# Kernel tuning notes

Hardware: AMD Instinct MI355X
Metric: run time of the kernel (lower is better)

## Reference

```python
import jax, jax.numpy as jnp
import numpy as np

B, S, D, H, BLK = 2, 4096, 1024, 16, 64

def setup_inputs() -> dict:
    key = jax.random.key(0)
    ks = jax.random.split(key, 6)
    sc = 0.02
    nb = S // BLK
    g_tok = 128
    ng = g_tok // BLK
    n_mid = nb - ng - 2
    return {
        "tokens": jax.random.normal(ks[0], (B, S, D), dtype=jnp.float32),
        "band_mask": jnp.ones((B, 1, n_mid, BLK, 3 * BLK), dtype=jnp.float32),
        "from_mask": jnp.ones((B, 1, S, 1), dtype=jnp.float32),
        "to_mask": jnp.ones((B, 1, 1, S), dtype=jnp.float32),
        "Wq": jax.random.normal(ks[1], (D, D), dtype=jnp.float32) * sc,
        "Wk": jax.random.normal(ks[2], (D, D), dtype=jnp.float32) * sc,
        "Wv": jax.random.normal(ks[3], (D, D), dtype=jnp.float32) * sc,
        "Wu": jax.random.normal(ks[4], (D, D), dtype=jnp.float32) * sc,
        "bu": jnp.zeros((D,), dtype=jnp.float32),
        "num_global_tokens": 128,
    }

def _forward(tokens, band_mask, from_mask, to_mask, Wq, Wk, Wv, Wu, bu, g):
    b, s, dm = tokens.shape
    h, blk = H, BLK
    d = dm // h
    nb = s // blk
    ng = g // blk
    rs = 1.0 / (d ** 0.5)
    pen = -10000.0

    def heads(x):
        return x.reshape(b, s, h, d).transpose(0, 2, 1, 3)  # (b,h,s,d)

    q = heads(tokens @ Wq)
    k = heads(tokens @ Wk)
    v = heads(tokens @ Wv)
    bq = q.reshape(b, h, nb, blk, d)
    bk = k.reshape(b, h, nb, blk, d)
    bv = v.reshape(b, h, nb, blk, d)

    # --- global (first) block rows: attend to everything ---
    fp = jnp.einsum('bhqd,bhkd->bhqk', q[:, :, :g], k) * rs + (1.0 - to_mask) * pen
    fw = jax.nn.softmax(fp, axis=-1)
    first = jnp.einsum('bhqk,bhkd->bhqd', fw, v).reshape(b, h, ng, blk, d)

    # --- second block: global keys + first 3 non-global blocks ---
    q1 = min(3, nb - ng)
    st = ng * blk
    k2 = jnp.concatenate([k[:, :, :g], k[:, :, st:st + q1 * blk]], axis=2)
    v2 = jnp.concatenate([v[:, :, :g], v[:, :, st:st + q1 * blk]], axis=2)
    p2 = jnp.einsum('bhqd,bhkd->bhqk', bq[:, :, ng], k2) * rs
    p2 = p2 + (1.0 - to_mask[:, :, :, :blk * (ng + q1)]) * pen
    c2 = jnp.einsum('bhqk,bhkd->bhqd', jax.nn.softmax(p2, axis=-1), v2)[:, :, None]

    # --- middle blocks: sliding window (prev, self, next) + global keys ---
    m = nb - ng - 2
    ek = jnp.concatenate([bk[:, :, ng:ng + m], bk[:, :, ng + 1:ng + 1 + m],
                          bk[:, :, ng + 2:ng + 2 + m]], axis=3)  # (b,h,m,3*blk,d)
    ev = jnp.concatenate([bv[:, :, ng:ng + m], bv[:, :, ng + 1:ng + 1 + m],
                          bv[:, :, ng + 2:ng + 2 + m]], axis=3)
    mq = bq[:, :, ng + 1:ng + 1 + m]  # (b,h,m,blk,d)
    inner = jnp.einsum('bhmqd,bhmkd->bhmqk', mq, ek) * rs + (1.0 - band_mask) * pen
    fb = jnp.einsum('bhmqd,bhkd->bhmqk', mq, k[:, :, :g]) * rs
    fb = fb + (1.0 - to_mask[:, :, :, :g][:, :, :, None, :]) * pen
    aw = jax.nn.softmax(jnp.concatenate([fb, inner], axis=-1), axis=-1)
    cm = (jnp.einsum('bhmqk,bhmkd->bhmqd', aw[..., g:], ev)
          + jnp.einsum('bhmqk,bhkd->bhmqd', aw[..., :g], v[:, :, :g]))

    # --- last block: global keys + last 3 blocks ---
    ql = min(3, nb - ng)
    kl = jnp.concatenate([k[:, :, :g], k[:, :, -(ql * blk):]], axis=2)
    vl = jnp.concatenate([v[:, :, :g], v[:, :, -(ql * blk):]], axis=2)
    lm = jnp.concatenate([to_mask[:, :, :, :g], to_mask[:, :, :, -(ql * blk):]], axis=3)
    pl = jnp.einsum('bhqd,bhkd->bhqk', bq[:, :, -1], kl) * rs + (1.0 - lm) * pen
    cl = jnp.einsum('bhqk,bhkd->bhqd', jax.nn.softmax(pl, axis=-1), vl)[:, :, None]

    ctx = jnp.concatenate([first, c2, cm, cl], axis=2).reshape(b, h, s, d) * from_mask
    ctx = ctx.transpose(0, 2, 1, 3).reshape(b, s, dm)
    return ctx @ Wu + bu

def reference(tokens, band_mask, from_mask, to_mask, Wq, Wk, Wv, Wu, bu, num_global_tokens):
    return _forward(tokens, band_mask, from_mask, to_mask, Wq, Wk, Wv, Wu, bu, num_global_tokens)
```

## Files before the change

### kernel.cpp

```cpp
#include <hip/hip_runtime.h>

typedef unsigned short u16;
using bfrag = __attribute__((ext_vector_type(8))) short;
using f32x4 = __attribute__((ext_vector_type(4))) float;

#define PEN  (-10000.0f)
#define RSC  (0.125f)

__device__ __forceinline__ u16 f2bf(float f) {
  union { float f; unsigned u; } v; v.f = f;
  unsigned r = v.u + 0x7fffu + ((v.u >> 16) & 1u);
  return (u16)(r >> 16);
}

__device__ __forceinline__ void gload16(const u16* g, u16* l) {
  __builtin_amdgcn_global_load_lds(
      (const __attribute__((address_space(1))) unsigned int*)g,
      (__attribute__((address_space(3))) unsigned int*)l, 16, 0, 0);
}

__global__ __launch_bounds__(256) void prep_k(
    const float* __restrict__ tokens, u16* __restrict__ tok_bf,
    const float* __restrict__ w0, const float* __restrict__ w1,
    const float* __restrict__ w2, const float* __restrict__ w3,
    u16* __restrict__ wt) {
  __shared__ float tile[64][65];
  int id = blockIdx.x, t = threadIdx.x;
  if (id < 8192) {
    int i = id * 256 + t;
    float4 v = ((const float4*)tokens)[i];
    u16 o[4] = { f2bf(v.x), f2bf(v.y), f2bf(v.z), f2bf(v.w) };
    *(uint2*)(tok_bf + (size_t)i * 4) = *(uint2*)o;
    return;
  }
  int wid = id - 8192;
  int z = wid >> 8, rem = wid & 255;
  const float* W = (z == 0) ? w0 : (z == 1) ? w1 : (z == 2) ? w2 : w3;
  u16* out = wt + (size_t)z * 1024 * 1024;
  int k0 = (rem & 15) * 64, n0 = (rem >> 4) * 64;
#pragma unroll
  for (int i = 0; i < 16; ++i) {
    int idx = i * 256 + t, kk = idx >> 6, nn = idx & 63;
    tile[nn][kk] = W[(size_t)(k0 + kk) * 1024 + n0 + nn];
  }
  __syncthreads();
#pragma unroll
  for (int i = 0; i < 16; ++i) {
    int idx = i * 256 + t, nn = idx >> 6, kk = idx & 63;
    out[(size_t)(n0 + nn) * 1024 + k0 + kk] = f2bf(tile[nn][kk]);
  }
}

__global__ __launch_bounds__(256) void gemm_qkv_k(
    const u16* __restrict__ A, const u16* __restrict__ WT,
    u16* __restrict__ Q, u16* __restrict__ K, u16* __restrict__ VT) {
  __shared__ alignas(16) u16 smem[17408];
  u16* As = smem;
  u16* Bs = smem + 8192;
  int t = threadIdx.x;
  int n0 = blockIdx.x * 128, r0 = blockIdx.y * 128;
  int wave = t >> 6, lane = t & 63, quad = lane >> 4, lcol = lane & 15;
  int wr = wave & 1, wc = wave >> 1;
  int rsel = lane >> 3;
  int sseg = (lane & 7) ^ rsel;
  f32x4 acc[4][4];
#pragma unroll
  for (int mt = 0; mt < 4; ++mt)
#pragma unroll
    for (int nt = 0; nt < 4; ++nt) acc[mt][nt] = (f32x4){0.f, 0.f, 0.f, 0.f};

  const u16* a0 = A + (size_t)r0 * 1024 + sseg * 8;
  const u16* b0 = WT + (size_t)n0 * 1024 + sseg * 8;
  int sw = lcol & 7;

  for (int kt = 0; kt < 16; ++kt) {
#pragma unroll
    for (int i = 0; i < 4; ++i) {
      int ii = wave * 4 + i;
      int row = ii * 8 + rsel;
      gload16(a0 + (size_t)row * 1024 + kt * 64, As + ii * 512);
      gload16(b0 + (size_t)row * 1024 + kt * 64, Bs + ii * 512);
    }
    __syncthreads();
#pragma unroll
    for (int kh = 0; kh < 2; ++kh) {
      int seg = ((kh * 4 + quad) ^ sw) * 8;
      bfrag af[4], bf[4];
#pragma unroll
      for (int x = 0; x < 4; ++x) {
        af[x] = *(const bfrag*)(As + (wr * 64 + x * 16 + lcol) * 64 + seg);
        bf[x] = *(const bfrag*)(Bs + (wc * 64 + x * 16 + lcol) * 64 + seg);
      }
#pragma unroll
      for (int mt = 0; mt < 4; ++mt)
#pragma unroll
        for (int nt = 0; nt < 4; ++nt)
          acc[mt][nt] = __builtin_amdgcn_mfma_f32_16x16x32_bf16(af[mt], bf[nt], acc[mt][nt], 0, 0, 0);
    }
    __syncthreads();
  }
  u16 (*Cs)[136] = (u16(*)[136])smem;
#pragma unroll
  for (int mt = 0; mt < 4; ++mt)
#pragma unroll
    for (int nt = 0; nt < 4; ++nt)
#pragma unroll
      for (int r = 0; r < 4; ++r)
        Cs[wr * 64 + mt * 16 + quad * 4 + r][wc * 64 + nt * 16 + lcol] = f2bf(acc[mt][nt][r]);
  __syncthreads();
  int which = n0 >> 10;
  int b = r0 >> 12, s0v = r0 & 4095;
  if (which < 2) {
    int row = t >> 1, seg = t & 1;
    int h = ((n0 & 1023) >> 6) + seg;
    u16* outp = (which == 0 ? Q : K) + (((size_t)(b * 16 + h) * 4096 + s0v + row) << 6);
#pragma unroll
    for (int jj = 0; jj < 8; ++jj)
      *(uint4*)(outp + jj * 8) = *(uint4*)&Cs[row][seg * 64 + jj * 8];
  } else {
    int c = t & 127, h = ((n0 & 1023) >> 6) + (c >> 6), d = c & 63;
    u16* vtrow = VT + ((size_t)(b * 16 + h) << 18) + ((size_t)d << 12) + s0v;
    int sgb = t >> 7;
#pragma unroll
    for (int i = 0; i < 8; ++i) {
      int sg = sgb + 2 * i;
      u16 tmp[8];
#pragma unroll
      for (int rr = 0; rr < 8; ++rr) tmp[rr] = Cs[sg * 8 + rr][c];
      *(uint4*)(vtrow + sg * 8) = *(uint4*)tmp;
    }
  }
}

__global__ __launch_bounds__(256) void attn_k(
    const u16* __restrict__ Qg, const u16* __restrict__ Kg, const u16* __restrict__ VTg,
    const float* __restrict__ band_mask, const float* __restrict__ from_mask,
    const float* __restrict__ to_mask, u16* __restrict__ ctx,
    float* __restrict__ Opart, float* __restrict__ lbuf) {
  __shared__ alignas(16) u16 QPs[4096];
  __shared__ alignas(16) u16 Ks[2][4096];
  __shared__ alignas(16) u16 VTs[2][4096];

  int t = threadIdx.x;
  int wave = t >> 6, lane = t & 63, quad = lane >> 4, lcol = lane & 15;
  int sw = lcol & 7;
  int bh = blockIdx.y, b = bh >> 4;
  bool is_band = blockIdx.x < 62;
  int j, chunk = 0, nit, sb = 0;
  if (is_band) {
    j = blockIdx.x + 2; nit = 5;
    sb = (j == 2) ? 2 : ((j == 63) ? 61 : j - 1);
  } else {
    int jc = blockIdx.x - 62; j = jc >> 3; chunk = jc & 7; nit = 8;
  }
  bool bandmask_blk = is_band && (j >= 3) && (j <= 62);

  int srow0 = t >> 3, srow1 = 32 + srow0, sseg = t & 7;
  int lds0 = srow0 * 64 + ((sseg ^ (srow0 & 7)) << 3);
  int lds1 = srow1 * 64 + ((sseg ^ (srow1 & 7)) << 3);
  const u16* kbase = Kg + (((size_t)bh * 4096) << 6) + sseg * 8;
  const u16* vbase = VTg + ((size_t)bh << 18) + sseg * 8;

  auto kb_of = [&](int it) {
    return is_band ? ((it < 2) ? it : (sb + it - 2)) : (chunk * 8 + it);
  };

  uint4 kr0, kr1, vr0, vr1;
  auto load_tile = [&](int kb) {
    kr0 = *(const uint4*)(kbase + (((size_t)kb * 64 + srow0) << 6));
    kr1 = *(const uint4*)(kbase + (((size_t)kb * 64 + srow1) << 6));
    vr0 = *(const uint4*)(vbase + ((size_t)srow0 << 12) + kb * 64);
    vr1 = *(const uint4*)(vbase + ((size_t)srow1 << 12) + kb * 64);
  };
  auto write_tile = [&](int buf) {
    *(uint4*)&Ks[buf][lds0] = kr0;  *(uint4*)&Ks[buf][lds1] = kr1;
    *(uint4*)&VTs[buf][lds0] = vr0; *(uint4*)&VTs[buf][lds1] = vr1;
  };

  {
    const u16* qsrc = Qg + (((size_t)bh * 4096 + j * 64) << 6) + sseg * 8;
    uint4 q0 = *(const uint4*)(qsrc + srow0 * 64);
    uint4 q1 = *(const uint4*)(qsrc + srow1 * 64);
    *(uint4*)&QPs[lds0] = q0; *(uint4*)&QPs[lds1] = q1;
    load_tile(kb_of(0));
    write_tile(0);
  }

  float l_part[4] = {0.f, 0.f, 0.f, 0.f};
  f32x4 oa[4];
#pragma unroll
  for (int nt = 0; nt < 4; ++nt) oa[nt] = (f32x4){0.f, 0.f, 0.f, 0.f};
  bfrag qf[2];

  int poff = lcol & 7;
  int hb = lcol >> 3;
  int q1_4 = (quad & 1) * 4;

  for (int it = 0; it < nit; ++it) {
    int buf = it & 1;
    if (it > 0) write_tile(buf);
    if (it + 1 < nit) load_tile(kb_of(it + 1));
    __syncthreads();
    if (it == 0) {
#pragma unroll
      for (int kh = 0; kh < 2; ++kh)
        qf[kh] = *(const bfrag*)&QPs[(wave * 16 + lcol) * 64 + (((kh * 4 + quad) ^ sw) << 3)];
    }
    int kb = kb_of(it);

    f32x4 sc[4];
#pragma unroll
    for (int nt = 0; nt < 4; ++nt) sc[nt] = (f32x4){0.f, 0.f, 0.f, 0.f};
#pragma unroll
    for (int kh = 0; kh < 2; ++kh) {
      int seg = ((kh * 4 + quad) ^ sw) << 3;
#pragma unroll
      for (int nt = 0; nt < 4; ++nt) {
        bfrag kf = *(const bfrag*)&Ks[buf][(nt * 16 + lcol) * 64 + seg];
        sc[nt] = __builtin_amdgcn_mfma_f32_16x16x32_bf16(qf[kh], kf, sc[nt], 0, 0, 0);
      }
    }

    bool use_band = bandmask_blk && (it >= 2);
    if (!use_band) {
#pragma unroll
      for (int nt = 0; nt < 4; ++nt) {
        float tm = to_mask[b * 4096 + kb * 64 + nt * 16 + lcol];
        float pn = (1.0f - tm) * PEN;
#pragma unroll
        for (int r = 0; r < 4; ++r) {
          float p = __expf(sc[nt][r] * RSC + pn);
          l_part[r] += p;
          int pseg = (nt * 2 + hb) ^ (q1_4 + r);
          QPs[(wave * 16 + quad * 4 + r) * 64 + pseg * 8 + poff] = f2bf(p);
        }
      }
    } else {
      const float* bm = band_mask + (((size_t)b * 60 + (j - 3)) << 6) * 192 + (it - 2) * 64;
#pragma unroll
      for (int r = 0; r < 4; ++r) {
        int qrow = wave * 16 + quad * 4 + r;
#pragma unroll
        for (int nt = 0; nt < 4; ++nt) {
          float msk = bm[(size_t)qrow * 192 + nt * 16 + lcol];
          float p = __expf(sc[nt][r] * RSC + (1.0f - msk) * PEN);
          l_part[r] += p;
          int pseg = (nt * 2 + hb) ^ (q1_4 + r);
          QPs[qrow * 64 + pseg * 8 + poff] = f2bf(p);
        }
      }
    }

#pragma unroll
    for (int kh = 0; kh < 2; ++kh) {
      int seg = ((kh * 4 + quad) ^ sw) << 3;
      bfrag pf = *(const bfrag*)&QPs[(wave * 16 + lcol) * 64 + seg];
#pragma unroll
      for (int nt = 0; nt < 4; ++nt) {
        bfrag vf = *(const bfrag*)&VTs[buf][(nt * 16 + lcol) * 64 + seg];
        oa[nt] = __builtin_amdgcn_mfma_f32_16x16x32_bf16(pf, vf, oa[nt], 0, 0, 0);
      }
    }
  }

  if (is_band) {
    float sc_r[4];
#pragma unroll
    for (int r = 0; r < 4; ++r) {
#pragma unroll
      for (int d = 1; d < 16; d <<= 1) l_part[r] += __shfl_xor(l_part[r], d);
      int qrow = wave * 16 + quad * 4 + r;
      sc_r[r] = from_mask[b * 4096 + j * 64 + qrow] / l_part[r];
    }
#pragma unroll
    for (int nt = 0; nt < 4; ++nt)
#pragma unroll
      for (int r = 0; r < 4; ++r) {
        int pseg = (nt * 2 + hb) ^ (q1_4 + r);
        QPs[(wave * 16 + quad * 4 + r) * 64 + pseg * 8 + poff] = f2bf(oa[nt][r] * sc_r[r]);
      }
    __syncthreads();
    u16* dst = ctx + (((size_t)bh * 4096 + j * 64) << 6);
#pragma unroll
    for (int i = 0; i < 2; ++i) {
      int idx = i * 256 + t, row = idx >> 3, s = idx & 7;
      *(uint4*)(dst + row * 64 + s * 8) = *(uint4*)&QPs[row * 64 + ((s ^ (row & 7)) << 3)];
    }
  } else {
    size_t base = (((size_t)(bh * 2 + j) * 8 + chunk) << 6);
#pragma unroll
    for (int nt = 0; nt < 4; ++nt)
#pragma unroll
      for (int r = 0; r < 4; ++r) {
        int row = wave * 16 + quad * 4 + r;
        Opart[((base + row) << 6) + nt * 16 + lcol] = oa[nt][r];
      }
#pragma unroll
    for (int r = 0; r < 4; ++r) {
#pragma unroll
      for (int d = 1; d < 16; d <<= 1) l_part[r] += __shfl_xor(l_part[r], d);
    }
    if (lcol == 0) {
#pragma unroll
      for (int r = 0; r < 4; ++r)
        lbuf[base + wave * 16 + quad * 4 + r] = l_part[r];
    }
  }
}

__global__ __launch_bounds__(256) void attn_combine_k(
    const float* __restrict__ Opart, const float* __restrict__ lbuf,
    const float* __restrict__ from_mask, u16* __restrict__ ctx) {
  int blk = blockIdx.x;
  int bh = blk >> 1, j = blk & 1, b = bh >> 4;
  int t = threadIdx.x;
  int row = t >> 2, dseg = (t & 3) << 4;

  float lt = 0.0f;
  float acc[16];
#pragma unroll
  for (int u = 0; u < 16; ++u) acc[u] = 0.0f;
#pragma unroll
  for (int c = 0; c < 8; ++c) {
    size_t rbase = (((size_t)blk * 8 + c) << 6) + row;
    lt += lbuf[rbase];
    const float* op = Opart + (rbase << 6) + dseg;
#pragma unroll
    for (int u = 0; u < 4; ++u) {
      float4 v = *(const float4*)(op + u * 4);
      acc[u * 4 + 0] += v.x;
      acc[u * 4 + 1] += v.y;
      acc[u * 4 + 2] += v.z;
      acc[u * 4 + 3] += v.w;
    }
  }
  float inv = from_mask[b * 4096 + j * 64 + row] / lt;
  u16* dst = ctx + (((size_t)bh * 4096 + j * 64 + row) << 6) + dseg;
  u16 o[8];
#pragma unroll
  for (int u = 0; u < 8; ++u) o[u] = f2bf(acc[u] * inv);
  *(uint4*)dst = *(uint4*)o;
#pragma unroll
  for (int u = 0; u < 8; ++u) o[u] = f2bf(acc[8 + u] * inv);
  *(uint4*)(dst + 8) = *(uint4*)o;
}

__global__ __launch_bounds__(256) void gemm_out_k(
    const u16* __restrict__ ctx, const u16* __restrict__ WTu,
    const float* __restrict__ bu, float* __restrict__ out) {
  __shared__ alignas(16) u16 smem[16384];
  u16* As = smem;
  u16* Bs = smem + 8192;
  int t = threadIdx.x;
  int n0 = blockIdx.x * 128, r0 = blockIdx.y * 128;
  int wave = t >> 6, lane = t & 63, quad = lane >> 4, lcol = lane & 15;
  int wr = wave & 1, wc = wave >> 1;
  int b = r0 >> 12, s0 = r0 & 4095;
  int rsel = lane >> 3;
  int sseg = (lane & 7) ^ rsel;
  int sw = lcol & 7;
  f32x4 acc[4][4];
#pragma unroll
  for (int mt = 0; mt < 4; ++mt)
#pragma unroll
    for (int nt = 0; nt < 4; ++nt) acc[mt][nt] = (f32x4){0.f, 0.f, 0.f, 0.f};

  const u16* b0 = WTu + (size_t)n0 * 1024 + sseg * 8;
  for (int kt = 0; kt < 16; ++kt) {
    const u16* a0 = ctx + (((size_t)(b * 16 + kt) * 4096 + s0) << 6) + sseg * 8;
#pragma unroll
    for (int i = 0; i < 4; ++i) {
      int ii = wave * 4 + i;
      int row = ii * 8 + rsel;
      gload16(a0 + (size_t)row * 64, As + ii * 512);
      gload16(b0 + (size_t)row * 1024 + kt * 64, Bs + ii * 512);
    }
    __syncthreads();
#pragma unroll
    for (int kh = 0; kh < 2; ++kh) {
      int seg = ((kh * 4 + quad) ^ sw) * 8;
      bfrag af[4], bf[4];
#pragma unroll
      for (int x = 0; x < 4; ++x) {
        af[x] = *(const bfrag*)(As + (wr * 64 + x * 16 + lcol) * 64 + seg);
        bf[x] = *(const bfrag*)(Bs + (wc * 64 + x * 16 + lcol) * 64 + seg);
      }
#pragma unroll
      for (int mt = 0; mt < 4; ++mt)
#pragma unroll
        for (int nt = 0; nt < 4; ++nt)
          acc[mt][nt] = __builtin_amdgcn_mfma_f32_16x16x32_bf16(af[mt], bf[nt], acc[mt][nt], 0, 0, 0);
    }
    __syncthreads();
  }
#pragma unroll
  for (int nt = 0; nt < 4; ++nt) {
    int n = n0 + wc * 64 + nt * 16 + lcol;
    float bv = bu[n];
#pragma unroll
    for (int mt = 0; mt < 4; ++mt)
#pragma unroll
      for (int r = 0; r < 4; ++r)
        out[(size_t)(r0 + wr * 64 + mt * 16 + quad * 4 + r) * 1024 + n] = acc[mt][nt][r] + bv;
  }
}

extern "C" void kernel_launch(void* const* d_in, const int* in_sizes, int n_in,
                              void* d_out, int out_size, void* d_ws, size_t ws_size,
                              hipStream_t stream) {
  const float* tokens    = (const float*)d_in[0];
  const float* band_mask = (const float*)d_in[1];
  const float* from_mask = (const float*)d_in[2];
  const float* to_mask   = (const float*)d_in[3];
  const float* Wq = (const float*)d_in[4];
  const float* Wk = (const float*)d_in[5];
  const float* Wv = (const float*)d_in[6];
  const float* Wu = (const float*)d_in[7];
  const float* bu = (const float*)d_in[8];
  float* out = (float*)d_out;

  char* ws = (char*)d_ws;
  u16* tok_bf = (u16*)(ws);
  u16* WT     = (u16*)(ws + 16777216);
  u16* Qb     = (u16*)(ws + 16777216 + 8388608);
  u16* Kb     = Qb + 8388608;
  u16* VTb    = Kb + 8388608;
  u16* ctx    = VTb + 8388608;
  float* Opart = (float*)(ctx + 8388608);
  float* lb    = Opart + (size_t)32 * 2 * 8 * 64 * 64;

  prep_k<<<9216, 256, 0, stream>>>(tokens, tok_bf, Wq, Wk, Wv, Wu, WT);
  gemm_qkv_k<<<dim3(24, 64), 256, 0, stream>>>(tok_bf, WT, Qb, Kb, VTb);
  attn_k<<<dim3(78, 32), 256, 0, stream>>>(Qb, Kb, VTb, band_mask, from_mask, to_mask,
                                           ctx, Opart, lb);
  attn_combine_k<<<64, 256, 0, stream>>>(Opart, lb, from_mask, ctx);
  gemm_out_k<<<dim3(8, 64), 256, 0, stream>>>(ctx, WT + (size_t)3 * 1024 * 1024, bu, out);
}
```

Measured before the change: 263.4 us.

## Use XOR-swizzled epilogue staging in QKV GEMM and narrower output GEMM tiles

The QKV GEMM epilogue now stages the bf16 results in two XOR-swizzled 64-column halves that reuse the As/Bs buffers, replacing the padded 136-wide array. This cuts shared memory per block and avoids LDS bank conflicts on both the row stores and the V-transpose reads. The output GEMM drops from 128x128 to 128x64 tiles, doubling the grid to 1024 blocks to fill more CUs and using fewer accumulator registers. The price is less reuse of each loaded tile in the output GEMM and more index arithmetic in the epilogue.

```diff
diff --git a/kernel.cpp b/kernel.cpp
--- a/kernel.cpp
+++ b/kernel.cpp
@@ -54,7 +54,7 @@
 __global__ __launch_bounds__(256) void gemm_qkv_k(
     const u16* __restrict__ A, const u16* __restrict__ WT,
     u16* __restrict__ Q, u16* __restrict__ K, u16* __restrict__ VT) {
-  __shared__ alignas(16) u16 smem[17408];
+  __shared__ alignas(16) u16 smem[16384];
   u16* As = smem;
   u16* Bs = smem + 8192;
   int t = threadIdx.x;
@@ -99,34 +99,45 @@
     }
     __syncthreads();
   }
-  u16 (*Cs)[136] = (u16(*)[136])smem;
-#pragma unroll
-  for (int mt = 0; mt < 4; ++mt)
-#pragma unroll
-    for (int nt = 0; nt < 4; ++nt)
-#pragma unroll
-      for (int r = 0; r < 4; ++r)
-        Cs[wr * 64 + mt * 16 + quad * 4 + r][wc * 64 + nt * 16 + lcol] = f2bf(acc[mt][nt][r]);
+  {
+    int poff = lcol & 7, hb = lcol >> 3, q1_4 = (quad & 1) * 4;
+    u16* half = wc ? Bs : As;
+#pragma unroll
+    for (int mt = 0; mt < 4; ++mt)
+#pragma unroll
+      for (int nt = 0; nt < 4; ++nt)
+#pragma unroll
+        for (int r = 0; r < 4; ++r) {
+          int row = wr * 64 + mt * 16 + quad * 4 + r;
+          int pseg = (nt * 2 + hb) ^ (q1_4 + r);
+          half[row * 64 + pseg * 8 + poff] = f2bf(acc[mt][nt][r]);
+        }
+  }
   __syncthreads();
   int which = n0 >> 10;
   int b = r0 >> 12, s0v = r0 & 4095;
   if (which < 2) {
     int row = t >> 1, seg = t & 1;
+    const u16* hsrc = seg ? Bs : As;
     int h = ((n0 & 1023) >> 6) + seg;
     u16* outp = (which == 0 ? Q : K) + (((size_t)(b * 16 + h) * 4096 + s0v + row) << 6);
 #pragma unroll
     for (int jj = 0; jj < 8; ++jj)
-      *(uint4*)(outp + jj * 8) = *(uint4*)&Cs[row][seg * 64 + jj * 8];
+      *(uint4*)(outp + jj * 8) = *(const uint4*)(hsrc + row * 64 + ((jj ^ (row & 7)) << 3));
   } else {
-    int c = t & 127, h = ((n0 & 1023) >> 6) + (c >> 6), d = c & 63;
-    u16* vtrow = VT + ((size_t)(b * 16 + h) << 18) + ((size_t)d << 12) + s0v;
+    int c = t & 127, h = ((n0 & 1023) >> 6) + (c >> 6);
+    int c_in = c & 63, cs = c_in >> 3, coff = c & 7;
+    const u16* hsrc = (c >> 6) ? Bs : As;
+    u16* vtrow = VT + ((size_t)(b * 16 + h) << 18) + ((size_t)(c_in & 63) << 12) + s0v;
+    vtrow = VT + ((size_t)(b * 16 + h) << 18) + ((size_t)c_in << 12) + s0v;
     int sgb = t >> 7;
 #pragma unroll
     for (int i = 0; i < 8; ++i) {
       int sg = sgb + 2 * i;
       u16 tmp[8];
 #pragma unroll
-      for (int rr = 0; rr < 8; ++rr) tmp[rr] = Cs[sg * 8 + rr][c];
+      for (int rr = 0; rr < 8; ++rr)
+        tmp[rr] = hsrc[(sg * 8 + rr) * 64 + ((cs ^ rr) << 3) + coff];
       *(uint4*)(vtrow + sg * 8) = *(uint4*)tmp;
     }
   }
@@ -348,20 +359,19 @@
 __global__ __launch_bounds__(256) void gemm_out_k(
     const u16* __restrict__ ctx, const u16* __restrict__ WTu,
     const float* __restrict__ bu, float* __restrict__ out) {
-  __shared__ alignas(16) u16 smem[16384];
+  __shared__ alignas(16) u16 smem[12288];
   u16* As = smem;
   u16* Bs = smem + 8192;
   int t = threadIdx.x;
-  int n0 = blockIdx.x * 128, r0 = blockIdx.y * 128;
+  int n0 = blockIdx.x * 64, r0 = blockIdx.y * 128;
   int wave = t >> 6, lane = t & 63, quad = lane >> 4, lcol = lane & 15;
-  int wr = wave & 1, wc = wave >> 1;
   int b = r0 >> 12, s0 = r0 & 4095;
   int rsel = lane >> 3;
   int sseg = (lane & 7) ^ rsel;
   int sw = lcol & 7;
-  f32x4 acc[4][4];
-#pragma unroll
-  for (int mt = 0; mt < 4; ++mt)
+  f32x4 acc[2][4];
+#pragma unroll
+  for (int mt = 0; mt < 2; ++mt)
 #pragma unroll
     for (int nt = 0; nt < 4; ++nt) acc[mt][nt] = (f32x4){0.f, 0.f, 0.f, 0.f};
 
@@ -369,24 +379,28 @@
   for (int kt = 0; kt < 16; ++kt) {
     const u16* a0 = ctx + (((size_t)(b * 16 + kt) * 4096 + s0) << 6) + sseg * 8;
 #pragma unroll
-    for (int i = 0; i < 4; ++i) {
-      int ii = wave * 4 + i;
-      int row = ii * 8 + rsel;
-      gload16(a0 + (size_t)row * 64, As + ii * 512);
-      gload16(b0 + (size_t)row * 1024 + kt * 64, Bs + ii * 512);
+    for (int i = 0; i < 6; ++i) {
+      int ii = wave * 6 + i;
+      if (ii < 16) {
+        gload16(a0 + (size_t)(ii * 8 + rsel) * 64, As + ii * 512);
+      } else {
+        int bi = ii - 16;
+        gload16(b0 + (size_t)(bi * 8 + rsel) * 1024 + kt * 64, Bs + bi * 512);
+      }
     }
     __syncthreads();
 #pragma unroll
     for (int kh = 0; kh < 2; ++kh) {
       int seg = ((kh * 4 + quad) ^ sw) * 8;
-      bfrag af[4], bf[4];
-#pragma unroll
-      for (int x = 0; x < 4; ++x) {
-        af[x] = *(const bfrag*)(As + (wr * 64 + x * 16 + lcol) * 64 + seg);
-        bf[x] = *(const bfrag*)(Bs + (wc * 64 + x * 16 + lcol) * 64 + seg);
-      }
-#pragma unroll
-      for (int mt = 0; mt < 4; ++mt)
+      bfrag af[2], bf[4];
+#pragma unroll
+      for (int x = 0; x < 2; ++x)
+        af[x] = *(const bfrag*)(As + (wave * 32 + x * 16 + lcol) * 64 + seg);
+#pragma unroll
+      for (int x = 0; x < 4; ++x)
+        bf[x] = *(const bfrag*)(Bs + (x * 16 + lcol) * 64 + seg);
+#pragma unroll
+      for (int mt = 0; mt < 2; ++mt)
 #pragma unroll
         for (int nt = 0; nt < 4; ++nt)
           acc[mt][nt] = __builtin_amdgcn_mfma_f32_16x16x32_bf16(af[mt], bf[nt], acc[mt][nt], 0, 0, 0);
@@ -395,13 +409,13 @@
   }
 #pragma unroll
   for (int nt = 0; nt < 4; ++nt) {
-    int n = n0 + wc * 64 + nt * 16 + lcol;
+    int n = n0 + nt * 16 + lcol;
     float bv = bu[n];
 #pragma unroll
-    for (int mt = 0; mt < 4; ++mt)
+    for (int mt = 0; mt < 2; ++mt)
 #pragma unroll
       for (int r = 0; r < 4; ++r)
-        out[(size_t)(r0 + wr * 64 + mt * 16 + quad * 4 + r) * 1024 + n] = acc[mt][nt][r] + bv;
+        out[(size_t)(r0 + wave * 32 + mt * 16 + quad * 4 + r) * 1024 + n] = acc[mt][nt][r] + bv;
   }
 }
 
@@ -434,5 +448,5 @@
   attn_k<<<dim3(78, 32), 256, 0, stream>>>(Qb, Kb, VTb, band_mask, from_mask, to_mask,
                                            ctx, Opart, lb);
   attn_combine_k<<<64, 256, 0, stream>>>(Opart, lb, from_mask, ctx);
-  gemm_out_k<<<dim3(8, 64), 256, 0, stream>>>(ctx, WT + (size_t)3 * 1024 * 1024, bu, out);
-}
+  gemm_out_k<<<dim3(16, 64), 256, 0, stream>>>(ctx, WT + (size_t)3 * 1024 * 1024, bu, out);
+}
```

New measurement: 268.2 us. No clear change (+1.8%).

## Shrink QKV GEMM LDS with swizzled epilogue, split launch, widen combine grid

Applied to the files above, without the earlier changes.

The QKV GEMM epilogue now stages the bf16 output tile in the existing A/B LDS halves using an XOR-swizzled layout instead of a padded 136-wide buffer. This cuts shared memory to 32KB, which may allow more resident blocks, and the swizzle is meant to reduce bank conflicts. The QKV GEMM is also split into two launches over row halves via a row offset, which adds launch overhead. The attention combine kernel now uses four times as many blocks, each handling 16 rows with 4 columns per thread, to spread a small reduction over more CUs.

```diff
diff --git a/kernel.cpp b/kernel.cpp
--- a/kernel.cpp
+++ b/kernel.cpp
@@ -53,12 +53,12 @@
 
 __global__ __launch_bounds__(256) void gemm_qkv_k(
     const u16* __restrict__ A, const u16* __restrict__ WT,
-    u16* __restrict__ Q, u16* __restrict__ K, u16* __restrict__ VT) {
-  __shared__ alignas(16) u16 smem[17408];
+    u16* __restrict__ Q, u16* __restrict__ K, u16* __restrict__ VT, int r_off) {
+  __shared__ alignas(16) u16 smem[16384];
   u16* As = smem;
   u16* Bs = smem + 8192;
   int t = threadIdx.x;
-  int n0 = blockIdx.x * 128, r0 = blockIdx.y * 128;
+  int n0 = blockIdx.x * 128, r0 = (blockIdx.y + r_off) * 128;
   int wave = t >> 6, lane = t & 63, quad = lane >> 4, lcol = lane & 15;
   int wr = wave & 1, wc = wave >> 1;
   int rsel = lane >> 3;
@@ -99,34 +99,44 @@
     }
     __syncthreads();
   }
-  u16 (*Cs)[136] = (u16(*)[136])smem;
-#pragma unroll
-  for (int mt = 0; mt < 4; ++mt)
-#pragma unroll
-    for (int nt = 0; nt < 4; ++nt)
-#pragma unroll
-      for (int r = 0; r < 4; ++r)
-        Cs[wr * 64 + mt * 16 + quad * 4 + r][wc * 64 + nt * 16 + lcol] = f2bf(acc[mt][nt][r]);
+  {
+    int poff = lcol & 7, hb = lcol >> 3, q1_4 = (quad & 1) * 4;
+    u16* half = wc ? Bs : As;
+#pragma unroll
+    for (int mt = 0; mt < 4; ++mt)
+#pragma unroll
+      for (int nt = 0; nt < 4; ++nt)
+#pragma unroll
+        for (int r = 0; r < 4; ++r) {
+          int row = wr * 64 + mt * 16 + quad * 4 + r;
+          int pseg = (nt * 2 + hb) ^ (q1_4 + r);
+          half[row * 64 + pseg * 8 + poff] = f2bf(acc[mt][nt][r]);
+        }
+  }
   __syncthreads();
   int which = n0 >> 10;
   int b = r0 >> 12, s0v = r0 & 4095;
   if (which < 2) {
     int row = t >> 1, seg = t & 1;
+    const u16* hsrc = seg ? Bs : As;
     int h = ((n0 & 1023) >> 6) + seg;
     u16* outp = (which == 0 ? Q : K) + (((size_t)(b * 16 + h) * 4096 + s0v + row) << 6);
 #pragma unroll
     for (int jj = 0; jj < 8; ++jj)
-      *(uint4*)(outp + jj * 8) = *(uint4*)&Cs[row][seg * 64 + jj * 8];
+      *(uint4*)(outp + jj * 8) = *(const uint4*)(hsrc + row * 64 + ((jj ^ (row & 7)) << 3));
   } else {
-    int c = t & 127, h = ((n0 & 1023) >> 6) + (c >> 6), d = c & 63;
-    u16* vtrow = VT + ((size_t)(b * 16 + h) << 18) + ((size_t)d << 12) + s0v;
+    int c = t & 127, h = ((n0 & 1023) >> 6) + (c >> 6);
+    int c_in = c & 63, cs = c_in >> 3, coff = c & 7;
+    const u16* hsrc = (c >> 6) ? Bs : As;
+    u16* vtrow = VT + ((size_t)(b * 16 + h) << 18) + ((size_t)c_in << 12) + s0v;
     int sgb = t >> 7;
 #pragma unroll
     for (int i = 0; i < 8; ++i) {
       int sg = sgb + 2 * i;
       u16 tmp[8];
 #pragma unroll
-      for (int rr = 0; rr < 8; ++rr) tmp[rr] = Cs[sg * 8 + rr][c];
+      for (int rr = 0; rr < 8; ++rr)
+        tmp[rr] = hsrc[(sg * 8 + rr) * 64 + ((cs ^ rr) << 3) + coff];
       *(uint4*)(vtrow + sg * 8) = *(uint4*)tmp;
     }
   }
@@ -311,38 +321,22 @@
 __global__ __launch_bounds__(256) void attn_combine_k(
     const float* __restrict__ Opart, const float* __restrict__ lbuf,
     const float* __restrict__ from_mask, u16* __restrict__ ctx) {
-  int blk = blockIdx.x;
-  int bh = blk >> 1, j = blk & 1, b = bh >> 4;
+  int unit = blockIdx.x >> 2, sub = blockIdx.x & 3;
+  int bh = unit >> 1, j = unit & 1, b = bh >> 4;
   int t = threadIdx.x;
-  int row = t >> 2, dseg = (t & 3) << 4;
-
-  float lt = 0.0f;
-  float acc[16];
-#pragma unroll
-  for (int u = 0; u < 16; ++u) acc[u] = 0.0f;
+  int row = sub * 16 + (t >> 4);
+  int dcol = (t & 15) * 4;
+  float lt = 0.0f, a0 = 0.f, a1 = 0.f, a2 = 0.f, a3 = 0.f;
 #pragma unroll
   for (int c = 0; c < 8; ++c) {
-    size_t rbase = (((size_t)blk * 8 + c) << 6) + row;
+    size_t rbase = (((size_t)unit * 8 + c) << 6) + row;
     lt += lbuf[rbase];
-    const float* op = Opart + (rbase << 6) + dseg;
-#pragma unroll
-    for (int u = 0; u < 4; ++u) {
-      float4 v = *(const float4*)(op + u * 4);
-      acc[u * 4 + 0] += v.x;
-      acc[u * 4 + 1] += v.y;
-      acc[u * 4 + 2] += v.z;
-      acc[u * 4 + 3] += v.w;
-    }
+    float4 v = *(const float4*)(Opart + (rbase << 6) + dcol);
+    a0 += v.x; a1 += v.y; a2 += v.z; a3 += v.w;
   }
   float inv = from_mask[b * 4096 + j * 64 + row] / lt;
-  u16* dst = ctx + (((size_t)bh * 4096 + j * 64 + row) << 6) + dseg;
-  u16 o[8];
-#pragma unroll
-  for (int u = 0; u < 8; ++u) o[u] = f2bf(acc[u] * inv);
-  *(uint4*)dst = *(uint4*)o;
-#pragma unroll
-  for (int u = 0; u < 8; ++u) o[u] = f2bf(acc[8 + u] * inv);
-  *(uint4*)(dst + 8) = *(uint4*)o;
+  u16 o[4] = { f2bf(a0 * inv), f2bf(a1 * inv), f2bf(a2 * inv), f2bf(a3 * inv) };
+  *(uint2*)(ctx + (((size_t)bh * 4096 + j * 64 + row) << 6) + dcol) = *(uint2*)o;
 }
 
 __global__ __launch_bounds__(256) void gemm_out_k(
@@ -430,9 +424,10 @@
   float* lb    = Opart + (size_t)32 * 2 * 8 * 64 * 64;
 
   prep_k<<<9216, 256, 0, stream>>>(tokens, tok_bf, Wq, Wk, Wv, Wu, WT);
-  gemm_qkv_k<<<dim3(24, 64), 256, 0, stream>>>(tok_bf, WT, Qb, Kb, VTb);
+  gemm_qkv_k<<<dim3(24, 32), 256, 0, stream>>>(tok_bf, WT, Qb, Kb, VTb, 0);
+  gemm_qkv_k<<<dim3(24, 32), 256, 0, stream>>>(tok_bf, WT, Qb, Kb, VTb, 32);
   attn_k<<<dim3(78, 32), 256, 0, stream>>>(Qb, Kb, VTb, band_mask, from_mask, to_mask,
                                            ctx, Opart, lb);
-  attn_combine_k<<<64, 256, 0, stream>>>(Opart, lb, from_mask, ctx);
+  attn_combine_k<<<256, 256, 0, stream>>>(Opart, lb, from_mask, ctx);
   gemm_out_k<<<dim3(8, 64), 256, 0, stream>>>(ctx, WT + (size_t)3 * 1024 * 1024, bu, out);
 }
```

Measured after the change: 260.8 us. No clear change (-1.0%).
